# Kernel tuning notes

Hardware: AMD Instinct MI355X
Metric: run time of the kernel (lower is better)

Reference implementation:

```python
import jax, jax.numpy as jnp
import numpy as np

B, NX, NC, C, H = 4, 1024, 2048, 1024, 16
DH = C // H            # head_dim = 64
SCALE = DH ** -0.5


def setup_inputs() -> dict:
    key = jax.random.key(0)
    ks = jax.random.split(key, 6)
    # sorted unique token indices to update per batch (== positions where update_mask==1)
    rng = np.random.default_rng(0)
    idx = np.stack([np.sort(rng.permutation(NC)[:NX]) for _ in range(B)]).astype(np.int32)
    return {
        "x": jax.random.normal(ks[0], (B, NX, C), jnp.float32),
        "update_idx": jnp.asarray(idx),                              # (B, NX) int32
        "cache_k": jax.random.normal(ks[1], (B, H, NC, DH), jnp.float32),
        "cache_v": jax.random.normal(ks[2], (B, H, NC, DH), jnp.float32),
        "w_qkv": jax.random.normal(ks[3], (3 * C, C), jnp.float32) * 0.02,
        "b_qkv": jnp.zeros((3 * C,), jnp.float32),
        "w_proj": jax.random.normal(ks[4], (C, C), jnp.float32) * 0.02,
        "b_proj": jnp.zeros((C,), jnp.float32),
    }


def reference(x, update_idx, cache_k, cache_v, w_qkv, b_qkv, w_proj, b_proj):
    Bq, N, Cq = x.shape
    # QKV projection: (B, N, 3C) -> (3, B, H, N, Dh) layout as in torch permute(2,0,3,1,4)
    qkv = (x @ w_qkv.T + b_qkv).reshape(Bq, N, 3, H, DH)
    q = qkv[:, :, 0].transpose(0, 2, 1, 3)  # (B, H, N, Dh)
    k = qkv[:, :, 1].transpose(0, 2, 1, 3)
    v = qkv[:, :, 2].transpose(0, 2, 1, 3)
    # masked_scatter_ of k/v into cache at the masked (updated) token slots.
    # Indices are sorted, so row-order masked_scatter == indexed scatter.
    scat = jax.vmap(lambda cache, idx, src: cache.at[:, idx, :].set(src))
    k_full = scat(cache_k, update_idx, k)    # (B, H, NC, Dh)
    v_full = scat(cache_v, update_idx, v)
    # plain attention: q scaled, full softmax over cache length
    attn = jax.nn.softmax(jnp.einsum('bhqd,bhkd->bhqk', q * SCALE, k_full), axis=-1)
    out = jnp.einsum('bhqk,bhkd->bhqd', attn, v_full)  # (B, H, N, Dh)
    out = out.transpose(0, 2, 1, 3).reshape(Bq, N, Cq)
    return out @ w_proj.T + b_proj
```

## Files before the change

kernel.cpp:

```cpp
#include <hip/hip_runtime.h>
#include <hip/hip_bf16.h>

#define B_   4
#define NX_  1024
#define NC_  2048
#define C_   1024
#define H_   16
#define DH_  64

typedef __attribute__((ext_vector_type(8))) __bf16 bf16x8;
typedef __attribute__((ext_vector_type(4))) float  f32x4;

static __device__ __forceinline__ unsigned short f2bf(float f) {
    unsigned int u = __float_as_uint(f);
    u += 0x7fffu + ((u >> 16) & 1u);
    return (unsigned short)(u >> 16);
}

static __device__ __forceinline__ unsigned int pk2(float lo, float hi) {
    unsigned int a = __float_as_uint(lo) + 0x8000u;
    unsigned int b = __float_as_uint(hi) + 0x8000u;
    return __builtin_amdgcn_perm(b, a, 0x07060302);
}

static __device__ __forceinline__ bf16x8 ldfrag(const unsigned short* p) {
    union { uint4 u; bf16x8 b; } cv;
    cv.u = *reinterpret_cast<const uint4*>(p);
    return cv.b;
}

static __device__ __forceinline__ bf16x8 asbf(uint4 u) {
    union { uint4 u; bf16x8 b; } cv;
    cv.u = u;
    return cv.b;
}

__global__ __launch_bounds__(256) void cvt_all_kernel(
    const float* __restrict__ x,  const float* __restrict__ wq,
    const float* __restrict__ wp, const float* __restrict__ ck,
    const float* __restrict__ cv_,
    unsigned short* __restrict__ xbf,  unsigned short* __restrict__ wqbf,
    unsigned short* __restrict__ wpbf, unsigned short* __restrict__ kfb,
    unsigned short* __restrict__ vt) {
    int blk = blockIdx.x;
    if (blk < 16384) {
        const float* src; unsigned short* dst; int i;
        if (blk < 4096)      { src = x;  dst = xbf;  i = blk; }
        else if (blk < 7168) { src = wq; dst = wqbf; i = blk - 4096; }
        else if (blk < 8192) { src = wp; dst = wpbf; i = blk - 7168; }
        else                 { src = ck; dst = kfb;  i = blk - 8192; }
        int idx = i * 256 + threadIdx.x;
        float4 f = reinterpret_cast<const float4*>(src)[idx];
        ushort4 o;
        o.x = f2bf(f.x); o.y = f2bf(f.y); o.z = f2bf(f.z); o.w = f2bf(f.w);
        reinterpret_cast<ushort4*>(dst)[idx] = o;
    } else {
        int i   = blk - 16384;
        int t   = threadIdx.x;
        int bh  = i >> 6;
        int kg  = i & 63;
        int d   = t & 63;
        int kci = t >> 6;
        int kc  = kg * 4 + kci;
        const float* src = cv_ + ((size_t)bh * NC_ + (size_t)kc * 8) * DH_ + d;
        union { uint4 u; unsigned short s[8]; } o;
#pragma unroll
        for (int j = 0; j < 8; j++) o.s[j] = f2bf(src[(size_t)j * DH_]);
        *reinterpret_cast<uint4*>(vt + ((size_t)bh * DH_ + d) * NC_ + (size_t)kc * 8) = o.u;
    }
}

#define LSTR 40

__global__ __launch_bounds__(256, 3) void qkv_gemm_kernel(
    const unsigned short* __restrict__ xbf,
    const unsigned short* __restrict__ wbf,
    const float* __restrict__ bias,
    const int* __restrict__ uidx,
    unsigned short* __restrict__ qb,
    unsigned short* __restrict__ kf,
    unsigned short* __restrict__ vt)
{
    __shared__ unsigned short As[128 * LSTR], Bs[128 * LSTR];
    __shared__ int jtab[128];
    int bn = blockIdx.x, bm = blockIdx.y;
    int w = threadIdx.x >> 6, l = threadIdx.x & 63;
    int quad = l >> 4, col = l & 15;
    int wr = w >> 1, wc = w & 1;
    int srow = w * 32 + (l >> 2), schk = (l & 3) * 8;

    const unsigned short* Ap = xbf + (size_t)(bm * 128 + srow) * C_ + schk;
    const unsigned short* Bp = wbf + (size_t)(bn * 128 + srow) * C_ + schk;
    unsigned short* Aw = As + srow * LSTR + schk;
    unsigned short* Bw = Bs + srow * LSTR + schk;

    f32x4 acc[4][4];
#pragma unroll
    for (int a = 0; a < 4; a++)
#pragma unroll
        for (int b = 0; b < 4; b++) acc[a][b] = (f32x4){0.f, 0.f, 0.f, 0.f};

    uint4 ar0, ar1, br0, br1;
#define LDREG(kk_)                                                       \
    {   int kk = (kk_) * 32;                                             \
        ar0 = *reinterpret_cast<const uint4*>(Ap + kk);                  \
        ar1 = *reinterpret_cast<const uint4*>(Ap + 16 * C_ + kk);        \
        br0 = *reinterpret_cast<const uint4*>(Bp + kk);                  \
        br1 = *reinterpret_cast<const uint4*>(Bp + 16 * C_ + kk);        \
    }
#define WRTILE()                                                         \
    {   *reinterpret_cast<uint4*>(Aw)             = ar0;                 \
        *reinterpret_cast<uint4*>(Aw + 16 * LSTR) = ar1;                 \
        *reinterpret_cast<uint4*>(Bw)             = br0;                 \
        *reinterpret_cast<uint4*>(Bw + 16 * LSTR) = br1;                 \
    }

    LDREG(0);
    WRTILE();
    LDREG(1);
    __syncthreads();
#pragma unroll 1
    for (int it = 0; it < 32; it++) {
        bf16x8 af[4], bfr[4];
#pragma unroll
        for (int t = 0; t < 4; t++) af[t]  = ldfrag(&As[(wr * 64 + t * 16 + col) * LSTR + quad * 8]);
#pragma unroll
        for (int t = 0; t < 4; t++) bfr[t] = ldfrag(&Bs[(wc * 64 + t * 16 + col) * LSTR + quad * 8]);
#pragma unroll
        for (int mt = 0; mt < 4; mt++)
#pragma unroll
            for (int nt = 0; nt < 4; nt++)
                acc[mt][nt] = __builtin_amdgcn_mfma_f32_16x16x32_bf16(af[mt], bfr[nt], acc[mt][nt], 0, 0, 0);
        if (it < 31) {
            __syncthreads();
            WRTILE();
            LDREG(it + 2 < 31 ? it + 2 : 31);
            __syncthreads();
        }
    }
#undef LDREG
#undef WRTILE

    int part = bn >> 3;
    float bv[4];
#pragma unroll
    for (int nt = 0; nt < 4; nt++) bv[nt] = bias[bn * 128 + wc * 64 + nt * 16 + col];

    if (part <= 1) {
        int nl[4];
#pragma unroll
        for (int nt = 0; nt < 4; nt++) nl[nt] = (bn * 128 + wc * 64 + nt * 16 + col) & 1023;
        const float QS = 0.18033688011112042f;
#pragma unroll
        for (int mt = 0; mt < 4; mt++)
#pragma unroll
            for (int r = 0; r < 4; r++) {
                int m = bm * 128 + wr * 64 + mt * 16 + quad * 4 + r;
                int b = m >> 10, i = m & 1023;
                int j = (part == 0) ? 0 : uidx[m];
#pragma unroll
                for (int nt = 0; nt < 4; nt++) {
                    int h = nl[nt] >> 6, d = nl[nt] & 63;
                    float v = acc[mt][nt][r] + bv[nt];
                    if (part == 0)
                        qb[((size_t)(b * H_ + h) * NX_ + i) * DH_ + d] = f2bf(v * QS);
                    else
                        kf[((size_t)(b * H_ + h) * NC_ + j) * DH_ + d] = f2bf(v);
                }
            }
    } else {
        if (threadIdx.x < 128) jtab[threadIdx.x] = uidx[bm * 128 + threadIdx.x];
        __syncthreads();
        int h = ((bn * 128 + wc * 64) & 1023) >> 6;
        int b = (bm * 128) >> 10;
        unsigned short* T = (wc == 0) ? As : Bs;
        int jv = jtab[wr * 64 + l];
        unsigned short* vb2 = vt + ((size_t)(b * H_ + h) * 64) * NC_ + jv;
#pragma unroll 1
        for (int round = 0; round < 2; round++) {
            if (wr == round) {
#pragma unroll
                for (int nt = 0; nt < 4; nt++)
#pragma unroll
                    for (int mt = 0; mt < 4; mt++) {
                        uint2 pk;
                        pk.x = pk2(acc[mt][nt][0] + bv[nt], acc[mt][nt][1] + bv[nt]);
                        pk.y = pk2(acc[mt][nt][2] + bv[nt], acc[mt][nt][3] + bv[nt]);
                        *reinterpret_cast<uint2*>(&T[(nt * 16 + col) * 72 + mt * 16 + quad * 4]) = pk;
                    }
                asm volatile("s_waitcnt lgkmcnt(0)" ::: "memory");
#pragma unroll 1
                for (int d = 0; d < 64; d++)
                    vb2[(size_t)d * NC_] = T[d * 72 + l];
            }
            __syncthreads();
        }
    }
}

#define PST 40
__global__ __launch_bounds__(256, 2) void attn_kernel(
    const unsigned short* __restrict__ qb,
    const unsigned short* __restrict__ kf,
    const unsigned short* __restrict__ vt,
    unsigned short* __restrict__ ao)
{
    __shared__ __align__(16) char smem[20480];
    unsigned short* Psh = (unsigned short*)smem;
    float* Om = (float*)smem;
    float* Lm = Om + 64 * 64;

    int id = blockIdx.x;
    int qt = (id >> 3) & 15;
    int bh = ((id >> 7) << 3) | (id & 7);
    int wave = threadIdx.x >> 6, lane = threadIdx.x & 63;
    int quad = lane >> 4, col = lane & 15;

    const unsigned short* qp = qb + ((size_t)bh * NX_ + qt * 64 + col) * DH_ + quad * 8;
    bf16x8 qf[4][2];
#pragma unroll
    for (int nt = 0; nt < 4; nt++) {
        qf[nt][0] = ldfrag(qp + nt * 16 * DH_);
        qf[nt][1] = ldfrag(qp + nt * 16 * DH_ + 32);
    }

    const unsigned short* Kp = kf + ((size_t)bh * NC_ + wave * 512 + col) * DH_ + quad * 8;
    const unsigned short* Vp = vt + ((size_t)bh * DH_ + col) * NC_ + wave * 512 + quad * 8;
    unsigned short* Pw = Psh + wave * (4 * 16 * PST);

    f32x4 o[4][4];
#pragma unroll
    for (int m = 0; m < 4; m++)
#pragma unroll
        for (int n = 0; n < 4; n++) o[m][n] = (f32x4){0.f, 0.f, 0.f, 0.f};
    float l_i[4] = {0.f, 0.f, 0.f, 0.f};

    uint4 ka[4], kn[4], vr[4];
#define LOADK(D, kb_) {                                                                  \
    const unsigned short* kp_ = Kp + (size_t)(kb_) * 32 * DH_;                           \
    D[0] = *reinterpret_cast<const uint4*>(kp_);                                         \
    D[1] = *reinterpret_cast<const uint4*>(kp_ + 32);                                    \
    D[2] = *reinterpret_cast<const uint4*>(kp_ + 16 * DH_);                              \
    D[3] = *reinterpret_cast<const uint4*>(kp_ + 16 * DH_ + 32); }
#define LOADV(kb_) {                                                                     \
    const unsigned short* vp_ = Vp + (size_t)(kb_) * 32;                                 \
    vr[0] = *reinterpret_cast<const uint4*>(vp_);                                        \
    vr[1] = *reinterpret_cast<const uint4*>(vp_ + 16 * NC_);                             \
    vr[2] = *reinterpret_cast<const uint4*>(vp_ + 32 * NC_);                             \
    vr[3] = *reinterpret_cast<const uint4*>(vp_ + 48 * NC_); }

    auto step = [&](const uint4 (&kc)[4]) {
#pragma unroll
        for (int nt = 0; nt < 4; nt++) {
            f32x4 s0 = (f32x4){0.f, 0.f, 0.f, 0.f};
            f32x4 s1 = (f32x4){0.f, 0.f, 0.f, 0.f};
            s0 = __builtin_amdgcn_mfma_f32_16x16x32_bf16(asbf(kc[0]), qf[nt][0], s0, 0, 0, 0);
            s0 = __builtin_amdgcn_mfma_f32_16x16x32_bf16(asbf(kc[1]), qf[nt][1], s0, 0, 0, 0);
            s1 = __builtin_amdgcn_mfma_f32_16x16x32_bf16(asbf(kc[2]), qf[nt][0], s1, 0, 0, 0);
            s1 = __builtin_amdgcn_mfma_f32_16x16x32_bf16(asbf(kc[3]), qf[nt][1], s1, 0, 0, 0);
            float p0 = exp2f(s0[0]), p1 = exp2f(s0[1]), p2 = exp2f(s0[2]), p3 = exp2f(s0[3]);
            float p4 = exp2f(s1[0]), p5 = exp2f(s1[1]), p6 = exp2f(s1[2]), p7 = exp2f(s1[3]);
            l_i[nt] += ((p0 + p1) + (p2 + p3)) + ((p4 + p5) + (p6 + p7));
            uint2 w0; w0.x = pk2(p0, p1); w0.y = pk2(p2, p3);
            uint2 w1; w1.x = pk2(p4, p5); w1.y = pk2(p6, p7);
            *reinterpret_cast<uint2*>(&Pw[nt * 16 * PST + col * PST +      quad * 4]) = w0;
            *reinterpret_cast<uint2*>(&Pw[nt * 16 * PST + col * PST + 16 + quad * 4]) = w1;
        }
        asm volatile("" ::: "memory");
#pragma unroll
        for (int nt = 0; nt < 4; nt++) {
            bf16x8 pf = ldfrag(&Pw[nt * 16 * PST + col * PST + quad * 8]);
            o[0][nt] = __builtin_amdgcn_mfma_f32_16x16x32_bf16(asbf(vr[0]), pf, o[0][nt], 0, 0, 0);
            o[1][nt] = __builtin_amdgcn_mfma_f32_16x16x32_bf16(asbf(vr[1]), pf, o[1][nt], 0, 0, 0);
            o[2][nt] = __builtin_amdgcn_mfma_f32_16x16x32_bf16(asbf(vr[2]), pf, o[2][nt], 0, 0, 0);
            o[3][nt] = __builtin_amdgcn_mfma_f32_16x16x32_bf16(asbf(vr[3]), pf, o[3][nt], 0, 0, 0);
        }
        asm volatile("" ::: "memory");
    };

    LOADK(ka, 0);
#pragma unroll 1
    for (int kb = 0; kb < 16; kb += 2) {
        LOADV(kb);
        LOADK(kn, kb + 1);
        step(ka);
        LOADV(kb + 1);
        int nx = (kb + 2 < 16) ? kb + 2 : 15;
        LOADK(ka, nx);
        step(kn);
    }
#undef LOADK
#undef LOADV

#pragma unroll
    for (int nt = 0; nt < 4; nt++) {
        l_i[nt] += __shfl_xor(l_i[nt], 16, 64);
        l_i[nt] += __shfl_xor(l_i[nt], 32, 64);
    }

    __syncthreads();
    if (wave == 3) {
#pragma unroll
        for (int mt = 0; mt < 4; mt++)
#pragma unroll
            for (int nt = 0; nt < 4; nt++)
#pragma unroll
                for (int r = 0; r < 4; r++)
                    Om[((mt * 4 + nt) * 4 + r) * 64 + lane] = o[mt][nt][r];
        if (quad == 0)
#pragma unroll
            for (int nt = 0; nt < 4; nt++) Lm[nt * 16 + col] = l_i[nt];
    }
    __syncthreads();
    if (wave == 2) {
#pragma unroll
        for (int mt = 0; mt < 4; mt++)
#pragma unroll
            for (int nt = 0; nt < 4; nt++)
#pragma unroll
                for (int r = 0; r < 4; r++)
                    Om[((mt * 4 + nt) * 4 + r) * 64 + lane] += o[mt][nt][r];
        if (quad == 0)
#pragma unroll
            for (int nt = 0; nt < 4; nt++) Lm[nt * 16 + col] += l_i[nt];
    }
    __syncthreads();
    if (wave == 1) {
#pragma unroll
        for (int mt = 0; mt < 4; mt++)
#pragma unroll
            for (int nt = 0; nt < 4; nt++)
#pragma unroll
                for (int r = 0; r < 4; r++)
                    Om[((mt * 4 + nt) * 4 + r) * 64 + lane] += o[mt][nt][r];
        if (quad == 0)
#pragma unroll
            for (int nt = 0; nt < 4; nt++) Lm[nt * 16 + col] += l_i[nt];
    }
    __syncthreads();
    if (wave == 0) {
        float inv[4];
#pragma unroll
        for (int nt = 0; nt < 4; nt++)
            inv[nt] = 1.f / (l_i[nt] + Lm[nt * 16 + col]);
        int b = bh >> 4, h = bh & 15;
#pragma unroll
        for (int mt = 0; mt < 4; mt++)
#pragma unroll
            for (int nt = 0; nt < 4; nt++) {
                int base = ((mt * 4 + nt) * 4) * 64 + lane;
                float v0 = (o[mt][nt][0] + Om[base      ]) * inv[nt];
                float v1 = (o[mt][nt][1] + Om[base +  64]) * inv[nt];
                float v2 = (o[mt][nt][2] + Om[base + 128]) * inv[nt];
                float v3 = (o[mt][nt][3] + Om[base + 192]) * inv[nt];
                int q = qt * 64 + nt * 16 + col;
                uint2 ov;
                ov.x = pk2(v0, v1);
                ov.y = pk2(v2, v3);
                *reinterpret_cast<uint2*>(ao + ((size_t)b * NX_ + q) * C_ +
                                          h * 64 + mt * 16 + quad * 4) = ov;
            }
    }
}

__global__ __launch_bounds__(256, 3) void proj_gemm_kernel(
    const unsigned short* __restrict__ abf,
    const unsigned short* __restrict__ wbf,
    const float* __restrict__ bias,
    float* __restrict__ out)
{
    __shared__ unsigned short As[128 * LSTR], Bs[64 * LSTR];
    int bn = blockIdx.x, bm = blockIdx.y;
    int w = threadIdx.x >> 6, l = threadIdx.x & 63;
    int quad = l >> 4, col = l & 15;
    int sarow = w * 32 + (l >> 2), sbrow = w * 16 + (l >> 2), schk = (l & 3) * 8;

    const unsigned short* Ap = abf + (size_t)(bm * 128 + sarow) * C_ + schk;
    const unsigned short* Bp = wbf + (size_t)(bn * 64 + sbrow) * C_ + schk;
    unsigned short* Aw = As + sarow * LSTR + schk;
    unsigned short* Bw = Bs + sbrow * LSTR + schk;

    f32x4 acc[2][4];
#pragma unroll
    for (int a = 0; a < 2; a++)
#pragma unroll
        for (int b = 0; b < 4; b++) acc[a][b] = (f32x4){0.f, 0.f, 0.f, 0.f};

    uint4 ar0, ar1, br0;
#define LDREG(kk_)                                                       \
    {   int kk = (kk_) * 32;                                             \
        ar0 = *reinterpret_cast<const uint4*>(Ap + kk);                  \
        ar1 = *reinterpret_cast<const uint4*>(Ap + 16 * C_ + kk);        \
        br0 = *reinterpret_cast<const uint4*>(Bp + kk);                  \
    }
#define WRTILE()                                                         \
    {   *reinterpret_cast<uint4*>(Aw)             = ar0;                 \
        *reinterpret_cast<uint4*>(Aw + 16 * LSTR) = ar1;                 \
        *reinterpret_cast<uint4*>(Bw)             = br0;                 \
    }

    LDREG(0);
    WRTILE();
    LDREG(1);
    __syncthreads();
#pragma unroll 1
    for (int it = 0; it < 32; it++) {
        bf16x8 af[2], bfr[4];
#pragma unroll
        for (int t = 0; t < 2; t++) af[t]  = ldfrag(&As[(w * 32 + t * 16 + col) * LSTR + quad * 8]);
#pragma unroll
        for (int t = 0; t < 4; t++) bfr[t] = ldfrag(&Bs[(t * 16 + col) * LSTR + quad * 8]);
#pragma unroll
        for (int mt = 0; mt < 2; mt++)
#pragma unroll
            for (int nt = 0; nt < 4; nt++)
                acc[mt][nt] = __builtin_amdgcn_mfma_f32_16x16x32_bf16(af[mt], bfr[nt], acc[mt][nt], 0, 0, 0);
        if (it < 31) {
            __syncthreads();
            WRTILE();
            LDREG(it + 2 < 31 ? it + 2 : 31);
            __syncthreads();
        }
    }
#undef LDREG
#undef WRTILE

    float bv[4];
#pragma unroll
    for (int nt = 0; nt < 4; nt++) bv[nt] = bias[bn * 64 + nt * 16 + col];
#pragma unroll
    for (int mt = 0; mt < 2; mt++)
#pragma unroll
        for (int r = 0; r < 4; r++) {
            int m = bm * 128 + w * 32 + mt * 16 + quad * 4 + r;
#pragma unroll
            for (int nt = 0; nt < 4; nt++) {
                int n = bn * 64 + nt * 16 + col;
                out[(size_t)m * C_ + n] = acc[mt][nt][r] + bv[nt];
            }
        }
}

extern "C" void kernel_launch(void* const* d_in, const int* in_sizes, int n_in,
                              void* d_out, int out_size, void* d_ws, size_t ws_size,
                              hipStream_t stream) {
    const float* x      = (const float*)d_in[0];
    const int*   uidx   = (const int*)  d_in[1];
    const float* cachek = (const float*)d_in[2];
    const float* cachev = (const float*)d_in[3];
    const float* wqkv   = (const float*)d_in[4];
    const float* bqkv   = (const float*)d_in[5];
    const float* wproj  = (const float*)d_in[6];
    const float* bproj  = (const float*)d_in[7];
    float* out = (float*)d_out;

    char* ws = (char*)d_ws;
    unsigned short* xbf  = (unsigned short*)(ws);
    unsigned short* wqbf = (unsigned short*)(ws + (8ull  << 20));
    unsigned short* wpbf = (unsigned short*)(ws + (14ull << 20));
    unsigned short* qb   = (unsigned short*)(ws + (16ull << 20));
    unsigned short* kfb  = (unsigned short*)(ws + (24ull << 20));
    unsigned short* vtb  = (unsigned short*)(ws + (40ull << 20));
    unsigned short* aob  = (unsigned short*)(ws + (56ull << 20));

    cvt_all_kernel<<<20480, 256, 0, stream>>>(x, wqkv, wproj, cachek, cachev,
                                              xbf, wqbf, wpbf, kfb, vtb);
    qkv_gemm_kernel <<<dim3(24, 32), 256, 0, stream>>>(xbf, wqbf, bqkv, uidx, qb, kfb, vtb);
    attn_kernel     <<<1024, 256, 0, stream>>>(qb, kfb, vtb, aob);
    proj_gemm_kernel<<<dim3(16, 32), 256, 0, stream>>>(aob, wpbf, bproj, out);
}
```

Measured before the change: 272.3 us.

## Stage K/V tiles via async global-to-LDS loads and keep P in registers

The attention kernel now double-buffers K and V tiles in shared memory using global_load_lds with block-wide syncs, instead of each wave loading its own K/V slice straight into registers. V's key order is permuted in the cvt and qkv kernels so that the exp'd scores, packed with v_cvt_pk_bf16_f32, can feed the PV MFMA directly from registers without a round-trip through LDS. Row sums are now computed with an MFMA against a ones vector rather than with scalar adds and shuffles. This adds LDS usage (64KB per block, which may cut occupancy) and per-tile __syncthreads, and it relies on the permuted V layout matching the MFMA operand layout.

```diff
diff --git a/kernel.cpp b/kernel.cpp
--- a/kernel.cpp
+++ b/kernel.cpp
@@ -23,17 +23,24 @@
     return __builtin_amdgcn_perm(b, a, 0x07060302);
 }
 
+static __device__ __forceinline__ unsigned int cvtpk(float lo, float hi) {
+    unsigned int r;
+    asm("v_cvt_pk_bf16_f32 %0, %1, %2" : "=v"(r) : "v"(lo), "v"(hi));
+    return r;
+}
+
 static __device__ __forceinline__ bf16x8 ldfrag(const unsigned short* p) {
     union { uint4 u; bf16x8 b; } cv;
     cv.u = *reinterpret_cast<const uint4*>(p);
     return cv.b;
 }
 
-static __device__ __forceinline__ bf16x8 asbf(uint4 u) {
-    union { uint4 u; bf16x8 b; } cv;
-    cv.u = u;
-    return cv.b;
-}
+#define AS1 __attribute__((address_space(1)))
+#define AS3 __attribute__((address_space(3)))
+static __device__ __forceinline__ void gload16(const unsigned short* g, unsigned short* l) {
+    __builtin_amdgcn_global_load_lds((const AS1 void*)g, (AS3 void*)l, 16, 0, 0);
+}
+
 
 __global__ __launch_bounds__(256) void cvt_all_kernel(
     const float* __restrict__ x,  const float* __restrict__ wq,
@@ -66,7 +73,13 @@
         union { uint4 u; unsigned short s[8]; } o;
 #pragma unroll
         for (int j = 0; j < 8; j++) o.s[j] = f2bf(src[(size_t)j * DH_]);
-        *reinterpret_cast<uint4*>(vt + ((size_t)bh * DH_ + d) * NC_ + (size_t)kc * 8) = o.u;
+        int m = kc & 3;
+        int pos0 = (m < 2) ? 4 * m : 4 * m - 7;
+        unsigned short* vb = vt + ((size_t)bh * DH_ + d) * NC_ + (kc >> 2) * 32 + pos0 * 4;
+        uint2 lo2; lo2.x = o.u.x; lo2.y = o.u.y;
+        uint2 hi2; hi2.x = o.u.z; hi2.y = o.u.w;
+        *reinterpret_cast<uint2*>(vb)     = lo2;
+        *reinterpret_cast<uint2*>(vb + 8) = hi2;
     }
 }
 
@@ -175,7 +188,10 @@
         int b = (bm * 128) >> 10;
         unsigned short* T = (wc == 0) ? As : Bs;
         int jv = jtab[wr * 64 + l];
-        unsigned short* vb2 = vt + ((size_t)(b * H_ + h) * 64) * NC_ + jv;
+        int c_ = (jv >> 2) & 7;
+        int sp = (c_ < 4) ? 2 * c_ : 2 * c_ - 7;
+        int jp = (jv & ~31) | (sp << 2) | (jv & 3);
+        unsigned short* vb2 = vt + ((size_t)(b * H_ + h) * 64) * NC_ + jp;
 #pragma unroll 1
         for (int round = 0; round < 2; round++) {
             if (wr == round) {
@@ -198,22 +214,20 @@
     }
 }
 
-#define PST 40
 __global__ __launch_bounds__(256, 2) void attn_kernel(
     const unsigned short* __restrict__ qb,
     const unsigned short* __restrict__ kf,
     const unsigned short* __restrict__ vt,
     unsigned short* __restrict__ ao)
 {
-    __shared__ __align__(16) char smem[20480];
-    unsigned short* Psh = (unsigned short*)smem;
-    float* Om = (float*)smem;
+    __shared__ __align__(16) unsigned short smem[2][16384];
+    float* Om = (float*)&smem[0][0];
     float* Lm = Om + 64 * 64;
 
     int id = blockIdx.x;
     int qt = (id >> 3) & 15;
     int bh = ((id >> 7) << 3) | (id & 7);
-    int wave = threadIdx.x >> 6, lane = threadIdx.x & 63;
+    int w = threadIdx.x >> 6, lane = threadIdx.x & 63;
     int quad = lane >> 4, col = lane & 15;
 
     const unsigned short* qp = qb + ((size_t)bh * NX_ + qt * 64 + col) * DH_ + quad * 8;
@@ -224,82 +238,100 @@
         qf[nt][1] = ldfrag(qp + nt * 16 * DH_ + 32);
     }
 
-    const unsigned short* Kp = kf + ((size_t)bh * NC_ + wave * 512 + col) * DH_ + quad * 8;
-    const unsigned short* Vp = vt + ((size_t)bh * DH_ + col) * NC_ + wave * 512 + quad * 8;
-    unsigned short* Pw = Psh + wave * (4 * 16 * PST);
+    const unsigned short* Kp = kf + ((size_t)bh * NC_ + w * 32 + (lane >> 2)) * DH_ + (lane & 3) * 8;
+    const unsigned short* Vp = vt + ((size_t)bh * DH_ + (lane >> 2)) * NC_ + w * 32 + (lane & 3) * 8;
 
     f32x4 o[4][4];
 #pragma unroll
     for (int m = 0; m < 4; m++)
 #pragma unroll
         for (int n = 0; n < 4; n++) o[m][n] = (f32x4){0.f, 0.f, 0.f, 0.f};
-    float l_i[4] = {0.f, 0.f, 0.f, 0.f};
-
-    uint4 ka[4], kn[4], vr[4];
-#define LOADK(D, kb_) {                                                                  \
-    const unsigned short* kp_ = Kp + (size_t)(kb_) * 32 * DH_;                           \
-    D[0] = *reinterpret_cast<const uint4*>(kp_);                                         \
-    D[1] = *reinterpret_cast<const uint4*>(kp_ + 32);                                    \
-    D[2] = *reinterpret_cast<const uint4*>(kp_ + 16 * DH_);                              \
-    D[3] = *reinterpret_cast<const uint4*>(kp_ + 16 * DH_ + 32); }
-#define LOADV(kb_) {                                                                     \
-    const unsigned short* vp_ = Vp + (size_t)(kb_) * 32;                                 \
-    vr[0] = *reinterpret_cast<const uint4*>(vp_);                                        \
-    vr[1] = *reinterpret_cast<const uint4*>(vp_ + 16 * NC_);                             \
-    vr[2] = *reinterpret_cast<const uint4*>(vp_ + 32 * NC_);                             \
-    vr[3] = *reinterpret_cast<const uint4*>(vp_ + 48 * NC_); }
-
-    auto step = [&](const uint4 (&kc)[4]) {
+    f32x4 lacc[4];
+#pragma unroll
+    for (int n = 0; n < 4; n++) lacc[n] = (f32x4){0.f, 0.f, 0.f, 0.f};
+    bf16x8 onef;
+    { union { unsigned int u[4]; bf16x8 b; } c1;
+      c1.u[0] = c1.u[1] = c1.u[2] = c1.u[3] = 0x3F803F80u; onef = c1.b; }
+
+    auto stage = [&](int bi, int t_) {
+        unsigned short* Kl = &smem[bi][w * 1024];
+        unsigned short* Kh = &smem[bi][4096 + w * 1024];
+        unsigned short* Vd = &smem[bi][8192 + w * 2048];
+        const unsigned short* kg = Kp + (size_t)t_ * (128 * DH_);
+        const unsigned short* vg = Vp + t_ * 128;
+        gload16(kg,                Kl);
+        gload16(kg + 16 * DH_,     Kl + 512);
+        gload16(kg + 32,           Kh);
+        gload16(kg + 16 * DH_ + 32, Kh + 512);
+        gload16(vg,                Vd);
+        gload16(vg + 16 * NC_,     Vd + 512);
+        gload16(vg + 32 * NC_,     Vd + 1024);
+        gload16(vg + 48 * NC_,     Vd + 1536);
+    };
+
+    auto compute = [&](int bi) {
+        const unsigned short* Kl = &smem[bi][0];
+        const unsigned short* Kh = &smem[bi][4096];
+        const unsigned short* Vv = &smem[bi][8192];
+        int kr0 = (w * 32 + col) * 32 + quad * 8;
+        bf16x8 ka0 = ldfrag(&Kl[kr0]);
+        bf16x8 kh0 = ldfrag(&Kh[kr0]);
+        bf16x8 ka1 = ldfrag(&Kl[kr0 + 512]);
+        bf16x8 kh1 = ldfrag(&Kh[kr0 + 512]);
+        bf16x8 vfr[4];
+#pragma unroll
+        for (int m4 = 0; m4 < 4; m4++)
+            vfr[m4] = ldfrag(&Vv[(w * 64 + m4 * 16 + col) * 32 + quad * 8]);
+        f32x4 s[2][4];
 #pragma unroll
         for (int nt = 0; nt < 4; nt++) {
-            f32x4 s0 = (f32x4){0.f, 0.f, 0.f, 0.f};
-            f32x4 s1 = (f32x4){0.f, 0.f, 0.f, 0.f};
-            s0 = __builtin_amdgcn_mfma_f32_16x16x32_bf16(asbf(kc[0]), qf[nt][0], s0, 0, 0, 0);
-            s0 = __builtin_amdgcn_mfma_f32_16x16x32_bf16(asbf(kc[1]), qf[nt][1], s0, 0, 0, 0);
-            s1 = __builtin_amdgcn_mfma_f32_16x16x32_bf16(asbf(kc[2]), qf[nt][0], s1, 0, 0, 0);
-            s1 = __builtin_amdgcn_mfma_f32_16x16x32_bf16(asbf(kc[3]), qf[nt][1], s1, 0, 0, 0);
-            float p0 = exp2f(s0[0]), p1 = exp2f(s0[1]), p2 = exp2f(s0[2]), p3 = exp2f(s0[3]);
-            float p4 = exp2f(s1[0]), p5 = exp2f(s1[1]), p6 = exp2f(s1[2]), p7 = exp2f(s1[3]);
-            l_i[nt] += ((p0 + p1) + (p2 + p3)) + ((p4 + p5) + (p6 + p7));
-            uint2 w0; w0.x = pk2(p0, p1); w0.y = pk2(p2, p3);
-            uint2 w1; w1.x = pk2(p4, p5); w1.y = pk2(p6, p7);
-            *reinterpret_cast<uint2*>(&Pw[nt * 16 * PST + col * PST +      quad * 4]) = w0;
-            *reinterpret_cast<uint2*>(&Pw[nt * 16 * PST + col * PST + 16 + quad * 4]) = w1;
+            s[0][nt] = (f32x4){0.f, 0.f, 0.f, 0.f};
+            s[1][nt] = (f32x4){0.f, 0.f, 0.f, 0.f};
+            s[0][nt] = __builtin_amdgcn_mfma_f32_16x16x32_bf16(ka0, qf[nt][0], s[0][nt], 0, 0, 0);
+            s[0][nt] = __builtin_amdgcn_mfma_f32_16x16x32_bf16(kh0, qf[nt][1], s[0][nt], 0, 0, 0);
+            s[1][nt] = __builtin_amdgcn_mfma_f32_16x16x32_bf16(ka1, qf[nt][0], s[1][nt], 0, 0, 0);
+            s[1][nt] = __builtin_amdgcn_mfma_f32_16x16x32_bf16(kh1, qf[nt][1], s[1][nt], 0, 0, 0);
         }
-        asm volatile("" ::: "memory");
+        bf16x8 pf[4];
 #pragma unroll
         for (int nt = 0; nt < 4; nt++) {
-            bf16x8 pf = ldfrag(&Pw[nt * 16 * PST + col * PST + quad * 8]);
-            o[0][nt] = __builtin_amdgcn_mfma_f32_16x16x32_bf16(asbf(vr[0]), pf, o[0][nt], 0, 0, 0);
-            o[1][nt] = __builtin_amdgcn_mfma_f32_16x16x32_bf16(asbf(vr[1]), pf, o[1][nt], 0, 0, 0);
-            o[2][nt] = __builtin_amdgcn_mfma_f32_16x16x32_bf16(asbf(vr[2]), pf, o[2][nt], 0, 0, 0);
-            o[3][nt] = __builtin_amdgcn_mfma_f32_16x16x32_bf16(asbf(vr[3]), pf, o[3][nt], 0, 0, 0);
+            float e0 = exp2f(s[0][nt][0]), e1 = exp2f(s[0][nt][1]);
+            float e2 = exp2f(s[0][nt][2]), e3 = exp2f(s[0][nt][3]);
+            float e4 = exp2f(s[1][nt][0]), e5 = exp2f(s[1][nt][1]);
+            float e6 = exp2f(s[1][nt][2]), e7 = exp2f(s[1][nt][3]);
+            union { unsigned int u[4]; bf16x8 b; } pw;
+            pw.u[0] = cvtpk(e0, e1); pw.u[1] = cvtpk(e2, e3);
+            pw.u[2] = cvtpk(e4, e5); pw.u[3] = cvtpk(e6, e7);
+            pf[nt] = pw.b;
         }
-        asm volatile("" ::: "memory");
+#pragma unroll
+        for (int nt = 0; nt < 4; nt++)
+            lacc[nt] = __builtin_amdgcn_mfma_f32_16x16x32_bf16(onef, pf[nt], lacc[nt], 0, 0, 0);
+#pragma unroll
+        for (int m4 = 0; m4 < 4; m4++)
+#pragma unroll
+            for (int nt = 0; nt < 4; nt++)
+                o[m4][nt] = __builtin_amdgcn_mfma_f32_16x16x32_bf16(vfr[m4], pf[nt], o[m4][nt], 0, 0, 0);
     };
 
-    LOADK(ka, 0);
+    stage(0, 0);
+    __syncthreads();
 #pragma unroll 1
-    for (int kb = 0; kb < 16; kb += 2) {
-        LOADV(kb);
-        LOADK(kn, kb + 1);
-        step(ka);
-        LOADV(kb + 1);
-        int nx = (kb + 2 < 16) ? kb + 2 : 15;
-        LOADK(ka, nx);
-        step(kn);
-    }
-#undef LOADK
-#undef LOADV
-
-#pragma unroll
-    for (int nt = 0; nt < 4; nt++) {
-        l_i[nt] += __shfl_xor(l_i[nt], 16, 64);
-        l_i[nt] += __shfl_xor(l_i[nt], 32, 64);
-    }
-
-    __syncthreads();
-    if (wave == 3) {
+    for (int t2 = 0; t2 < 8; t2++) {
+        int t = t2 << 1;
+        stage(1, t + 1);
+        compute(0);
+        __syncthreads();
+        if (t + 2 < 16) stage(0, t + 2);
+        compute(1);
+        __syncthreads();
+    }
+
+    float l_i[4];
+#pragma unroll
+    for (int nt = 0; nt < 4; nt++) l_i[nt] = lacc[nt][0];
+
+    if (w == 3) {
 #pragma unroll
         for (int mt = 0; mt < 4; mt++)
 #pragma unroll
@@ -312,7 +344,7 @@
             for (int nt = 0; nt < 4; nt++) Lm[nt * 16 + col] = l_i[nt];
     }
     __syncthreads();
-    if (wave == 2) {
+    if (w == 2) {
 #pragma unroll
         for (int mt = 0; mt < 4; mt++)
 #pragma unroll
@@ -325,7 +357,7 @@
             for (int nt = 0; nt < 4; nt++) Lm[nt * 16 + col] += l_i[nt];
     }
     __syncthreads();
-    if (wave == 1) {
+    if (w == 1) {
 #pragma unroll
         for (int mt = 0; mt < 4; mt++)
 #pragma unroll
@@ -338,7 +370,7 @@
             for (int nt = 0; nt < 4; nt++) Lm[nt * 16 + col] += l_i[nt];
     }
     __syncthreads();
-    if (wave == 0) {
+    if (w == 0) {
         float inv[4];
 #pragma unroll
         for (int nt = 0; nt < 4; nt++)
```

Measured after the change: 268.5 us. Within noise of the previous version (-1.4%).
